# Performance work log

Hardware: AMD Instinct MI355X
Metric: run time of the kernel (lower is better)

## Reference

```python
import jax, jax.numpy as jnp
import numpy as np

S = 64.0
M = 0.5
EPS = 1e-12  # F.normalize default eps


def setup_inputs() -> dict:
    key = jax.random.key(0)
    k1, k2, k3 = jax.random.split(key, 3)
    B, F, C = 512, 512, 85742
    feature = jax.random.normal(k1, (B, F), dtype=jnp.float32)
    header = jax.random.normal(k2, (F, C), dtype=jnp.float32)
    label = jax.random.randint(k3, (B,), 0, C, dtype=jnp.int64)
    return {"feature": feature, "header": header, "label": label}


def reference(feature, header, label):
    B = feature.shape[0]
    rows = jnp.arange(B)
    # per-row L2 normalize (torch F.normalize semantics)
    feat = feature / jnp.maximum(jnp.linalg.norm(feature, axis=-1, keepdims=True), EPS)
    logits = feat @ header  # (B, C)
    # per-row sum-of-abs normalization
    logits = logits / jnp.sum(jnp.abs(logits), axis=-1, keepdims=True)
    # arccos-margin injection at the target class
    t = logits[rows, label]
    t_m = jnp.cos(jnp.arccos(t) + M)
    logits = logits.at[rows, label].set(t_m)
    # loss_v = sum_b -(1/B) * log softmax(s*logits_b)[label_b]
    lse = jax.nn.logsumexp(S * logits, axis=-1)  # (B,)
    loss_v = jnp.mean(lse - S * t_m)
    return loss_v
```

## Files before the change

### kernel.cpp

```cpp
#include <hip/hip_runtime.h>
#include <math.h>


#define B_ROWS 512
#define K_DIM  512
#define C_COLS 85742
#define BN 64
#define BK 32
#define LDB 40
#define NKS (K_DIM / BK)
#define NREP 64

typedef float  f32x4  __attribute__((ext_vector_type(4)));
typedef short  bf16x8 __attribute__((ext_vector_type(8)));
typedef unsigned short u16x8 __attribute__((ext_vector_type(8)));
typedef unsigned int   u32x4 __attribute__((ext_vector_type(4)));

__device__ __forceinline__ unsigned short f2bf(float f) {
  unsigned int u = __float_as_uint(f);
  u += 0x7fffu + ((u >> 16) & 1u);
  return (unsigned short)(u >> 16);
}

__global__ __launch_bounds__(64)
void normalize_kernel(const float* __restrict__ feature,
                      unsigned short* __restrict__ feat_bf) {
  const int row  = blockIdx.x;
  const int lane = threadIdx.x;
  const float* src = feature + (size_t)row * K_DIM + lane * 8;
  f32x4 v0 = *(const f32x4*)src;
  f32x4 v1 = *(const f32x4*)(src + 4);
  float ss = v0[0]*v0[0] + v0[1]*v0[1] + v0[2]*v0[2] + v0[3]*v0[3]
           + v1[0]*v1[0] + v1[1]*v1[1] + v1[2]*v1[2] + v1[3]*v1[3];
  #pragma unroll
  for (int m = 1; m < 64; m <<= 1) ss += __shfl_xor(ss, m);
  const float scale = 1.0f / fmaxf(sqrtf(ss), 1e-12f);
  u16x8 o;
  o[0] = f2bf(v0[0] * scale); o[1] = f2bf(v0[1] * scale);
  o[2] = f2bf(v0[2] * scale); o[3] = f2bf(v0[3] * scale);
  o[4] = f2bf(v1[0] * scale); o[5] = f2bf(v1[1] * scale);
  o[6] = f2bf(v1[2] * scale); o[7] = f2bf(v1[3] * scale);
  *(u16x8*)(feat_bf + (size_t)row * K_DIM + lane * 8) = o;
}

__global__ __launch_bounds__(512, 4)
void gemm_moments_kernel(const float* __restrict__ header,
                         const unsigned short* __restrict__ feat_bf,
                         const long long* __restrict__ label,
                         float* __restrict__ moments_rep,
                         float* __restrict__ t_orig) {
  __shared__ unsigned short b_lds[2][BN * LDB];
  __shared__ int lds_label[B_ROWS];

  const int tid = threadIdx.x;
  const int c0  = blockIdx.x * BN;

  lds_label[tid] = (int)label[tid];

  const int wave = tid >> 6;
  const int lane = tid & 63;
  const int g    = lane >> 4;
  const int l16  = lane & 15;
  const int wrow = wave * 64;

  const bool stager = tid < 256;
  const int  c_l    = tid & 63;
  const int  w8     = (tid >> 6) * 8;
  const bool cok    = (c0 + c_l) < C_COLS;
  const int  cg     = cok ? (c0 + c_l) : 0;

  f32x4 acc[4][4] = {};
  float v[8];

  if (stager) {
    const float* p = header + (size_t)w8 * C_COLS + cg;
    #pragma unroll
    for (int j = 0; j < 8; ++j) v[j] = p[(size_t)j * C_COLS];
    #pragma unroll
    for (int j = 0; j < 8; ++j) if (!cok) v[j] = 0.f;
    u32x4 d;
    #pragma unroll
    for (int i = 0; i < 4; ++i)
      d[i] = ((unsigned int)f2bf(v[2*i+1]) << 16) | (unsigned int)f2bf(v[2*i]);
    *(u32x4*)&b_lds[0][c_l * LDB + w8] = d;
  }
  __syncthreads();

  for (int ks = 0; ks < NKS; ++ks) {
    const int  buf  = ks & 1;
    const bool more = (ks + 1) < NKS;

    bf16x8 afrag[4];
    #pragma unroll
    for (int mi = 0; mi < 4; ++mi)
      afrag[mi] = *(const bf16x8*)(feat_bf +
                   (size_t)(wrow + mi * 16 + l16) * K_DIM + ks * BK + g * 8);

    if (stager && more) {
      const float* p = header + ((size_t)(ks + 1) * BK + w8) * C_COLS + cg;
      #pragma unroll
      for (int j = 0; j < 8; ++j) v[j] = p[(size_t)j * C_COLS];
    }

    bf16x8 bfrag[4];
    #pragma unroll
    for (int ni = 0; ni < 4; ++ni)
      bfrag[ni] = *(const bf16x8*)&b_lds[buf][(ni * 16 + l16) * LDB + g * 8];

    #pragma unroll
    for (int mi = 0; mi < 4; ++mi)
      #pragma unroll
      for (int ni = 0; ni < 4; ++ni)
        acc[mi][ni] = __builtin_amdgcn_mfma_f32_16x16x32_bf16(
                        afrag[mi], bfrag[ni], acc[mi][ni], 0, 0, 0);

    if (stager && more) {
      #pragma unroll
      for (int j = 0; j < 8; ++j) if (!cok) v[j] = 0.f;
      u32x4 d;
      #pragma unroll
      for (int i = 0; i < 4; ++i)
        d[i] = ((unsigned int)f2bf(v[2*i+1]) << 16) | (unsigned int)f2bf(v[2*i]);
      *(u32x4*)&b_lds[buf ^ 1][c_l * LDB + w8] = d;
    }
    __syncthreads();
  }

  float* mrep = moments_rep + (size_t)(blockIdx.x & (NREP - 1)) * 5 * B_ROWS;
  #pragma unroll
  for (int mi = 0; mi < 4; ++mi) {
    #pragma unroll
    for (int r = 0; r < 4; ++r) {
      const int row = wrow + mi * 16 + g * 4 + r;
      const int lbl = lds_label[row];
      float sa = 0.f, s1 = 0.f, s2 = 0.f, s3 = 0.f, s4 = 0.f;
      #pragma unroll
      for (int ni = 0; ni < 4; ++ni) {
        const float x = acc[mi][ni][r];
        const int col = c0 + ni * 16 + l16;
        if (col == lbl) t_orig[row] = x;
        const float ax = fabsf(x), x2 = x * x;
        sa += ax; s1 += x; s2 += x2; s3 += x2 * x; s4 += x2 * x2;
      }
      #pragma unroll
      for (int m = 1; m < 16; m <<= 1) {
        sa += __shfl_xor(sa, m);
        s1 += __shfl_xor(s1, m);
        s2 += __shfl_xor(s2, m);
        s3 += __shfl_xor(s3, m);
        s4 += __shfl_xor(s4, m);
      }
      if (l16 == 0) {
        atomicAdd(&mrep[0 * B_ROWS + row], sa);
        atomicAdd(&mrep[1 * B_ROWS + row], s1);
        atomicAdd(&mrep[2 * B_ROWS + row], s2);
        atomicAdd(&mrep[3 * B_ROWS + row], s3);
        atomicAdd(&mrep[4 * B_ROWS + row], s4);
      }
    }
  }
}

__global__ __launch_bounds__(512)
void loss_kernel(const float* __restrict__ moments_rep,
                 const float* __restrict__ t_orig,
                 float* __restrict__ out) {
  const int r = threadIdx.x;
  double A = 0.0, S1 = 0.0, S2 = 0.0, S3 = 0.0, S4 = 0.0;
  #pragma unroll 4
  for (int b = 0; b < NREP; ++b) {
    const float* m = moments_rep + (size_t)b * 5 * B_ROWS;
    A  += (double)m[0 * B_ROWS + r];
    S1 += (double)m[1 * B_ROWS + r];
    S2 += (double)m[2 * B_ROWS + r];
    S3 += (double)m[3 * B_ROWS + r];
    S4 += (double)m[4 * B_ROWS + r];
  }
  const double to = (double)t_orig[r];
  const double z  = 64.0 / A;
  double sumexp = (double)C_COLS
                + z * (S1 + z * (0.5 * S2 + z * ((1.0/6.0) * S3 + z * (1.0/24.0) * S4)));
  double t = to / A;
  t = fmin(fmax(t, -1.0), 1.0);
  const double tm = cos(acos(t) + 0.5);
  sumexp += exp(64.0 * tm) - exp(z * to);
  double v = log(sumexp) - 64.0 * tm;

  #pragma unroll
  for (int m = 1; m < 64; m <<= 1) v += __shfl_xor(v, m);
  __shared__ double red[8];
  if ((r & 63) == 0) red[r >> 6] = v;
  __syncthreads();
  if (r == 0) {
    double tot = 0.0;
    #pragma unroll
    for (int i = 0; i < 8; ++i) tot += red[i];
    out[0] = (float)(tot / (double)B_ROWS);
  }
}

extern "C" void kernel_launch(void* const* d_in, const int* in_sizes, int n_in,
                              void* d_out, int out_size, void* d_ws, size_t ws_size,
                              hipStream_t stream) {
  const float*     feature = (const float*)d_in[0];
  const float*     header  = (const float*)d_in[1];
  const long long* label   = (const long long*)d_in[2];
  float* out = (float*)d_out;

  float* mrep   = (float*)d_ws;
  float* t_orig = mrep + NREP * 5 * B_ROWS;
  unsigned short* feat_bf = (unsigned short*)(t_orig + B_ROWS);

  hipMemsetAsync(d_ws, 0, (size_t)NREP * 5 * B_ROWS * sizeof(float), stream);
  normalize_kernel<<<B_ROWS, 64, 0, stream>>>(feature, feat_bf);
  const int nblocks = (C_COLS + BN - 1) / BN;
  gemm_moments_kernel<<<nblocks, 512, 0, stream>>>(header, feat_bf, label, mrep, t_orig);
  loss_kernel<<<1, 512, 0, stream>>>(mrep, t_orig, out);
}
```

Before: 361.8 us.

## Prefetch header two K-steps ahead and pre-pack features into MFMA fragment order

Header loads now run two K-steps ahead: the values already in registers are converted and written to the LDS double buffer before the MFMAs, and the next loads are issued right after. Scheduling barriers keep this ordering fixed. The normalize kernel also writes the bf16 features in per-wave, per-K-step fragment order, so A-fragment loads become contiguous and coalesced. The goal is to hide global-load latency on the memory-bound header stream, at the cost of keeping more data in flight and letting the compiler reorder less.

```diff
diff --git a/kernel.cpp b/kernel.cpp
--- a/kernel.cpp
+++ b/kernel.cpp
@@ -23,8 +23,8 @@
 }
 
 __global__ __launch_bounds__(64)
-void normalize_kernel(const float* __restrict__ feature,
-                      unsigned short* __restrict__ feat_bf) {
+void normalize_pack_kernel(const float* __restrict__ feature,
+                           unsigned short* __restrict__ featP) {
   const int row  = blockIdx.x;
   const int lane = threadIdx.x;
   const float* src = feature + (size_t)row * K_DIM + lane * 8;
@@ -40,12 +40,15 @@
   o[2] = f2bf(v0[2] * scale); o[3] = f2bf(v0[3] * scale);
   o[4] = f2bf(v1[0] * scale); o[5] = f2bf(v1[1] * scale);
   o[6] = f2bf(v1[2] * scale); o[7] = f2bf(v1[3] * scale);
-  *(u16x8*)(feat_bf + (size_t)row * K_DIM + lane * 8) = o;
+  const int w  = row >> 6, mi = (row >> 4) & 3, l16 = row & 15;
+  const int ks = lane >> 2, g  = lane & 3;
+  const size_t idx16 = (((size_t)w * 16 + ks) * 4 + mi) * 64 + g * 16 + l16;
+  *(u16x8*)(featP + idx16 * 8) = o;
 }
 
 __global__ __launch_bounds__(512, 4)
 void gemm_moments_kernel(const float* __restrict__ header,
-                         const unsigned short* __restrict__ feat_bf,
+                         const unsigned short* __restrict__ featP,
                          const long long* __restrict__ label,
                          float* __restrict__ moments_rep,
                          float* __restrict__ t_orig) {
@@ -73,34 +76,51 @@
   float v[8];
 
   if (stager) {
+    float u[8];
     const float* p = header + (size_t)w8 * C_COLS + cg;
     #pragma unroll
-    for (int j = 0; j < 8; ++j) v[j] = p[(size_t)j * C_COLS];
-    #pragma unroll
-    for (int j = 0; j < 8; ++j) if (!cok) v[j] = 0.f;
+    for (int j = 0; j < 8; ++j) u[j] = p[(size_t)j * C_COLS];
     u32x4 d;
     #pragma unroll
-    for (int i = 0; i < 4; ++i)
-      d[i] = ((unsigned int)f2bf(v[2*i+1]) << 16) | (unsigned int)f2bf(v[2*i]);
+    for (int i = 0; i < 4; ++i) {
+      const float a = cok ? u[2*i]   : 0.f;
+      const float b = cok ? u[2*i+1] : 0.f;
+      d[i] = ((unsigned int)f2bf(b) << 16) | (unsigned int)f2bf(a);
+    }
     *(u32x4*)&b_lds[0][c_l * LDB + w8] = d;
+    const float* p1 = header + ((size_t)BK + w8) * C_COLS + cg;
+    #pragma unroll
+    for (int j = 0; j < 8; ++j) v[j] = p1[(size_t)j * C_COLS];
   }
   __syncthreads();
 
   for (int ks = 0; ks < NKS; ++ks) {
-    const int  buf  = ks & 1;
-    const bool more = (ks + 1) < NKS;
+    const int buf = ks & 1;
 
     bf16x8 afrag[4];
     #pragma unroll
     for (int mi = 0; mi < 4; ++mi)
-      afrag[mi] = *(const bf16x8*)(feat_bf +
-                   (size_t)(wrow + mi * 16 + l16) * K_DIM + ks * BK + g * 8);
-
-    if (stager && more) {
-      const float* p = header + ((size_t)(ks + 1) * BK + w8) * C_COLS + cg;
+      afrag[mi] = *(const bf16x8*)(featP +
+                   ((((size_t)wave * 16 + ks) * 4 + mi) * 64 + lane) * 8);
+    __builtin_amdgcn_sched_barrier(0);
+
+    if (stager && ks + 1 < NKS) {
+      u32x4 d;
+      #pragma unroll
+      for (int i = 0; i < 4; ++i) {
+        const float a = cok ? v[2*i]   : 0.f;
+        const float b = cok ? v[2*i+1] : 0.f;
+        d[i] = ((unsigned int)f2bf(b) << 16) | (unsigned int)f2bf(a);
+      }
+      *(u32x4*)&b_lds[buf ^ 1][c_l * LDB + w8] = d;
+    }
+
+    if (stager && ks + 2 < NKS) {
+      const float* p = header + ((size_t)(ks + 2) * BK + w8) * C_COLS + cg;
       #pragma unroll
       for (int j = 0; j < 8; ++j) v[j] = p[(size_t)j * C_COLS];
     }
+    __builtin_amdgcn_sched_barrier(0);
 
     bf16x8 bfrag[4];
     #pragma unroll
@@ -114,15 +134,6 @@
         acc[mi][ni] = __builtin_amdgcn_mfma_f32_16x16x32_bf16(
                         afrag[mi], bfrag[ni], acc[mi][ni], 0, 0, 0);
 
-    if (stager && more) {
-      #pragma unroll
-      for (int j = 0; j < 8; ++j) if (!cok) v[j] = 0.f;
-      u32x4 d;
-      #pragma unroll
-      for (int i = 0; i < 4; ++i)
-        d[i] = ((unsigned int)f2bf(v[2*i+1]) << 16) | (unsigned int)f2bf(v[2*i]);
-      *(u32x4*)&b_lds[buf ^ 1][c_l * LDB + w8] = d;
-    }
     __syncthreads();
   }
 
@@ -209,11 +220,11 @@
 
   float* mrep   = (float*)d_ws;
   float* t_orig = mrep + NREP * 5 * B_ROWS;
-  unsigned short* feat_bf = (unsigned short*)(t_orig + B_ROWS);
+  unsigned short* featP = (unsigned short*)(t_orig + B_ROWS);
 
   hipMemsetAsync(d_ws, 0, (size_t)NREP * 5 * B_ROWS * sizeof(float), stream);
-  normalize_kernel<<<B_ROWS, 64, 0, stream>>>(feature, feat_bf);
+  normalize_pack_kernel<<<B_ROWS, 64, 0, stream>>>(feature, featP);
   const int nblocks = (C_COLS + BN - 1) / BN;
-  gemm_moments_kernel<<<nblocks, 512, 0, stream>>>(header, feat_bf, label, mrep, t_orig);
+  gemm_moments_kernel<<<nblocks, 512, 0, stream>>>(header, featP, label, mrep, t_orig);
   loss_kernel<<<1, 512, 0, stream>>>(mrep, t_orig, out);
 }
```

Measured after the change: 322.8 us. -10.8%, faster.
